# Kernel optimization log

Hardware: AMD Instinct MI355X
Metric: run time of the kernel (lower is better)

## Reference

```python
import jax, jax.numpy as jnp
import numpy as np

N, M, K, C, FF, H, OUT = 20000, 80000, 48, 64, 256, 4, 64


def _lin(x, w, b):
    return x @ w.T + b


def _bn(x, g, b, eps=1e-5):
    mu = x.mean(0)
    var = x.var(0)
    return (x - mu) * jax.lax.rsqrt(var + eps) * g + b


def setup_inputs() -> dict:
    key = jax.random.key(0)
    ks = jax.random.split(key, 24)
    voxel_features = jax.random.normal(ks[0], (M, C), jnp.float32)
    voxel_coords = jax.random.normal(ks[1], (M, 3), jnp.float32)
    query_coords = jax.random.normal(ks[2], (N, 3), jnp.float32)
    idx = jax.random.randint(ks[3], (N, K), 0, M)
    drop = jax.random.uniform(ks[4], (N, K)) < 0.1
    drop = drop.at[:, 0].set(False)  # keep >=1 valid key per query
    key_indices = jnp.where(drop, -1, idx)
    s = 0.05
    p = lambda i, shp: jax.random.normal(ks[i], shp, jnp.float32) * s
    return {
        "voxel_features": voxel_features,
        "voxel_coords": voxel_coords,
        "query_coords": query_coords,
        "key_indices": key_indices,
        "q_w": p(5, (C, 3)), "q_b": p(6, (C,)),
        "kpos_w": p(7, (C, 3)), "kpos_b": p(8, (C,)),
        "in_w": p(9, (3 * C, C)), "in_b": p(10, (3 * C,)),
        "out_w": p(11, (C, C)), "out_b": p(12, (C,)),
        "lin1_w": p(13, (FF, C)), "lin1_b": p(14, (FF,)),
        "lin2_w": p(15, (C, FF)), "lin2_b": p(16, (C,)),
        "norm_g": jnp.ones((C,), jnp.float32), "norm_b": jnp.zeros((C,), jnp.float32),
        "outl_w": p(17, (OUT, C)), "outl_b": p(18, (OUT,)),
        "obn_g": jnp.ones((OUT,), jnp.float32), "obn_b": jnp.zeros((OUT,), jnp.float32),
    }


def reference(voxel_features, voxel_coords, query_coords, key_indices,
              q_w, q_b, kpos_w, kpos_b, in_w, in_b, out_w, out_b,
              lin1_w, lin1_b, lin2_w, lin2_b, norm_g, norm_b,
              outl_w, outl_b, obn_g, obn_b):
    hd = C // H
    mask = key_indices < 0                      # (N,K) padded keys
    safe = jnp.where(mask, 0, key_indices)
    key_feats = voxel_features[safe]            # (N,K,C) hash-gather
    key_coords = voxel_coords[safe]             # (N,K,3)
    # query positional projection
    q_feat = jax.nn.relu(_lin(query_coords, q_w, q_b))          # (N,C)
    # relative coords + key positional conv1d(kernel=1) == linear on coord dim
    rel = key_coords - query_coords[:, None, :]                  # (N,K,3)
    key_feats = key_feats + jax.nn.relu(_lin(rel, kpos_w, kpos_b))
    # multihead attention, query length 1 per voxel
    Wq, Wk, Wv = jnp.split(in_w, 3, axis=0)
    bq, bk, bv = jnp.split(in_b, 3)
    q = (_lin(q_feat, Wq, bq) / jnp.sqrt(jnp.float32(hd))).reshape(N, H, hd)
    k = _lin(key_feats, Wk, bk).reshape(N, K, H, hd)
    v = _lin(key_feats, Wv, bv).reshape(N, K, H, hd)
    scores = jnp.einsum('nhd,nkhd->nhk', q, k)
    scores = jnp.where(mask[:, None, :], -jnp.inf, scores)
    attn = jax.nn.softmax(scores, axis=-1)
    ctx = jnp.einsum('nhk,nkhd->nhd', attn, v).reshape(N, C)
    att = _lin(ctx, out_w, out_b)                                # (N,C)
    # FFN + residual
    x = att + _lin(jax.nn.relu(_lin(att, lin1_w, lin1_b)), lin2_w, lin2_b)
    x = _bn(x, norm_g, norm_b)
    # output layer: Linear -> BN -> ReLU
    x = jax.nn.relu(_bn(_lin(x, outl_w, outl_b), obn_g, obn_b))
    return x
```

## Files before the change

kernel.cpp:

```cpp
#include <hip/hip_runtime.h>
#include <math.h>

#define N_Q 20000
#define KK 48
#define CC 64
#define FFD 256

#define TW_WOB   0
#define TW_WVT   4096
#define TW_L1B   8192
#define TW_L2B   16384
#define TW_OLB   24576
#define TW_QB    26624
#define TW_KB    28672
#define ST_OFF   32768
#define M_OFF    33024
#define VF_OFF   2593024
#define CTX_OFF  5153024

typedef short bf16x8 __attribute__((ext_vector_type(8)));
typedef float f32x4  __attribute__((ext_vector_type(4)));

__device__ __forceinline__ unsigned pk2(float a, float b) {
    unsigned r;
    asm("v_cvt_pk_bf16_f32 %0, %1, %2" : "=v"(r) : "v"(a), "v"(b));
    return r;
}
__device__ __forceinline__ unsigned f2bf(float a) {
    unsigned r;
    asm("v_cvt_pk_bf16_f32 %0, %1, 0" : "=v"(r) : "v"(a));
    return r & 0xffffu;
}
__device__ __forceinline__ float bflo(unsigned u) { return __uint_as_float(u << 16); }
__device__ __forceinline__ float bfhi(unsigned u) { return __uint_as_float(u & 0xffff0000u); }
__device__ __forceinline__ bf16x8 ldfrag(const unsigned short* p) {
    return *(const bf16x8*)p;
}

__global__ void prep_all(const float* __restrict__ in_w,
                         const float* __restrict__ out_w,
                         const float* __restrict__ lin1_w,
                         const float* __restrict__ lin2_w,
                         const float* __restrict__ outl_w,
                         const float* __restrict__ vfeat,
                         float* __restrict__ tw,
                         unsigned short* __restrict__ vfeat_bf,
                         float* __restrict__ stats)
{
    int t = blockIdx.x * 256 + threadIdx.x;
    unsigned* twu = (unsigned*)tw;
    if (t < 1280000) {
        float4 v = ((const float4*)vfeat)[t];
        uint2 p; p.x = pk2(v.x, v.y); p.y = pk2(v.z, v.w);
        ((uint2*)vfeat_bf)[t] = p;
    }
    if (t < 256) stats[t] = 0.0f;
    if (t < 4096) {
        if (t < 2048) {
            int p = t;
            int j2 = p & 3, lane = (p >> 2) & 63, nb = (p >> 8) & 3, ks = p >> 10;
            int nn = nb*16 + (lane & 15), k = ks*32 + (lane >> 4)*8 + 2*j2;
            twu[TW_WOB + p] = pk2(out_w[nn*64 + k], out_w[nn*64 + k + 1]);
        }
    } else if (t < 8192) {
        if (t < 6144) {
            int p = t - 4096;
            int j2 = p & 3, lane = (p >> 2) & 63, nb = (p >> 8) & 3, ks = p >> 10;
            int nn = nb*16 + (lane & 15), k = ks*32 + (lane >> 4)*8 + 2*j2;
            twu[TW_WVT + p] = pk2(in_w[(128 + nn)*64 + k], in_w[(128 + nn)*64 + k + 1]);
        }
    } else if (t < 16384) {
        int p = t - 8192;
        int j2 = p & 3, lane = (p >> 2) & 63, nb = (p >> 8) & 15, ks = p >> 12;
        int n = nb*16 + (lane & 15), k = ks*32 + (lane >> 4)*8 + 2*j2;
        twu[TW_L1B + p] = pk2(lin1_w[n*64 + k], lin1_w[n*64 + k + 1]);
    } else if (t < 24576) {
        int p = t - 16384;
        int j2 = p & 3, lane = (p >> 2) & 63, nb = (p >> 8) & 3, ks = p >> 10;
        int n = nb*16 + (lane & 15), k = ks*32 + (lane >> 4)*8 + 2*j2;
        twu[TW_L2B + p] = pk2(lin2_w[n*256 + k], lin2_w[n*256 + k + 1]);
    } else if (t < 26624) {
        int p = t - 24576;
        int j2 = p & 3, lane = (p >> 2) & 63, nb = (p >> 8) & 3, ks = p >> 10;
        int n = nb*16 + (lane & 15), k = ks*32 + (lane >> 4)*8 + 2*j2;
        twu[TW_OLB + p] = pk2(outl_w[n*64 + k], outl_w[n*64 + k + 1]);
    } else if (t < 28672) {
        int p = t - 26624;
        int j2 = p & 3, lane = (p >> 2) & 63, nb = (p >> 8) & 3, ks = p >> 10;
        int n = nb*16 + (lane & 15), k = ks*32 + (lane >> 4)*8 + 2*j2;
        twu[TW_QB + p] = pk2(in_w[n*64 + k], in_w[n*64 + k + 1]);
    } else if (t < 32768) {
        int p = t - 28672;
        int j2 = p & 3, lane = (p >> 2) & 63, nb = (p >> 8) & 3, h = p >> 10;
        int j = nb*16 + (lane & 15), k = (lane >> 4)*8 + 2*j2;
        unsigned u = 0;
        if (k < 16)
            u = pk2(in_w[(64 + h*16 + k)*64 + j], in_w[(64 + h*16 + k + 1)*64 + j]);
        twu[TW_KB + p] = u;
    }
}

__global__ __launch_bounds__(256) void m_kernel(
    const float* __restrict__ qcoord, const float* __restrict__ q_w,
    const float* __restrict__ q_b, const float* __restrict__ in_b,
    const float* __restrict__ tw, unsigned short* __restrict__ M_all)
{
    __shared__ __align__(16) unsigned short sQF[80*72];
    __shared__ __align__(16) unsigned short sQ[80*72];
    int t = threadIdx.x, base = blockIdx.x * 80;
    int colq = (t*4) & 63;
    float qwv[12];
    #pragma unroll
    for (int j = 0; j < 12; ++j) qwv[j] = q_w[colq*3 + j];
    float4 qb4 = *(const float4*)&q_b[colq];
    #pragma unroll
    for (int i = 0; i < 5; ++i) {
        int e = i*1024 + t*4, r = e >> 6, n = base + r;
        float c0 = qcoord[n*3], c1 = qcoord[n*3+1], c2 = qcoord[n*3+2];
        float f0 = fmaxf(fmaf(qwv[2],  c2, fmaf(qwv[1],  c1, fmaf(qwv[0], c0, qb4.x))), 0.f);
        float f1 = fmaxf(fmaf(qwv[5],  c2, fmaf(qwv[4],  c1, fmaf(qwv[3], c0, qb4.y))), 0.f);
        float f2 = fmaxf(fmaf(qwv[8],  c2, fmaf(qwv[7],  c1, fmaf(qwv[6], c0, qb4.z))), 0.f);
        float f3 = fmaxf(fmaf(qwv[11], c2, fmaf(qwv[10], c1, fmaf(qwv[9], c0, qb4.w))), 0.f);
        uint2 p; p.x = pk2(f0, f1); p.y = pk2(f2, f3);
        *(uint2*)&sQF[r*72 + colq] = p;
    }
    int w = t >> 6, lane = t & 63, l16 = lane & 15, quad = lane >> 4;
    const unsigned* QB = (const unsigned*)(tw + TW_QB);
    const unsigned* KB = (const unsigned*)(tw + TW_KB);
    bf16x8 qbf[2], kbf[4];
    #pragma unroll
    for (int ks = 0; ks < 2; ++ks)
        qbf[ks] = ldfrag((const unsigned short*)&QB[((ks*4 + w)*64 + lane)*4]);
    #pragma unroll
    for (int nb = 0; nb < 4; ++nb)
        kbf[nb] = ldfrag((const unsigned short*)&KB[((w*4 + nb)*64 + lane)*4]);
    __syncthreads();

    int cq = w*16 + l16;
    float bq = in_b[cq];
    #pragma unroll
    for (int mb = 0; mb < 5; ++mb) {
        bf16x8 a0 = ldfrag(&sQF[(mb*16 + l16)*72 + quad*8]);
        bf16x8 a1 = ldfrag(&sQF[(mb*16 + l16)*72 + 32 + quad*8]);
        f32x4 acc = {0.f, 0.f, 0.f, 0.f};
        acc = __builtin_amdgcn_mfma_f32_16x16x32_bf16(a0, qbf[0], acc, 0, 0, 0);
        acc = __builtin_amdgcn_mfma_f32_16x16x32_bf16(a1, qbf[1], acc, 0, 0, 0);
        #pragma unroll
        for (int reg = 0; reg < 4; ++reg) {
            int row = mb*16 + quad*4 + reg;
            sQ[row*72 + cq] = (unsigned short)f2bf((acc[reg] + bq) * 0.25f);
        }
    }
    #pragma unroll
    for (int mb = 0; mb < 5; ++mb) {
        bf16x8 a = {0,0,0,0,0,0,0,0};
        if (quad < 2) a = ldfrag(&sQ[(mb*16 + l16)*72 + w*16 + quad*8]);
        f32x4 acc[4];
        #pragma unroll
        for (int nb = 0; nb < 4; ++nb) {
            f32x4 z = {0.f, 0.f, 0.f, 0.f};
            acc[nb] = __builtin_amdgcn_mfma_f32_16x16x32_bf16(a, kbf[nb], z, 0, 0, 0);
        }
        #pragma unroll
        for (int nb = 0; nb < 4; ++nb)
            #pragma unroll
            for (int reg = 0; reg < 4; ++reg) {
                int r = base + mb*16 + quad*4 + reg, j = nb*16 + l16;
                M_all[(size_t)r*256 + w*64 + j] = (unsigned short)f2bf(acc[nb][reg]);
            }
    }
}

__global__ __launch_bounds__(256, 4) void attn_kernel(
    const unsigned short* __restrict__ vfeat_bf, const float* __restrict__ vcoord,
    const float* __restrict__ qcoord, const int* __restrict__ kidx,
    const float* __restrict__ kpos_w, const float* __restrict__ kpos_b,
    const float* __restrict__ in_b,
    const float* __restrict__ tw, const unsigned short* __restrict__ M_all,
    unsigned short* __restrict__ ctx_bf)
{
    __shared__ __align__(16) unsigned short skf2[4][KK*72];
    int wv = threadIdx.x >> 6, c = threadIdx.x & 63;
    int n = blockIdx.x * 4 + wv;
    unsigned short* skf = skf2[wv];
    int l16 = c & 15, quad = c >> 4;

    const unsigned short* Mrow = M_all + (size_t)n*256 + (l16 & 3)*64 + quad*8;
    bf16x8 mf0 = ldfrag(Mrow);
    bf16x8 mf1 = ldfrag(Mrow + 32);
    const unsigned* VBu = (const unsigned*)(tw + TW_WVT);
    bf16x8 wvf[2][4];
    #pragma unroll
    for (int ks = 0; ks < 2; ++ks)
        #pragma unroll
        for (int nb = 0; nb < 4; ++nb)
            wvf[ks][nb] = ldfrag((const unsigned short*)&VBu[((ks*4 + nb)*64 + c)*4]);

    float qc0 = qcoord[n*3+0], qc1 = qcoord[n*3+1], qc2 = qcoord[n*3+2];

    int kread = c < 48 ? c : 47;
    int idxv = kidx[(size_t)n*KK + kread];
    int sfe = idxv < 0 ? 0 : idxv;
    float rl0 = vcoord[sfe*3+0] - qc0;
    float rl1 = vcoord[sfe*3+1] - qc1;
    float rl2 = vcoord[sfe*3+2] - qc2;

    int o8 = c >> 3, jb8 = (c & 7) * 8;
    float w8[24], b8[8];
    #pragma unroll
    for (int q = 0; q < 6; ++q)
        *(float4*)&w8[q*4] = *(const float4*)(kpos_w + jb8*3 + q*4);
    *(float4*)&b8[0] = *(const float4*)(kpos_b + jb8);
    *(float4*)&b8[4] = *(const float4*)(kpos_b + jb8 + 4);

    uint4 fv[6];
    #pragma unroll
    for (int i = 0; i < 6; ++i) {
        int row = 8*i + o8;
        int si = __shfl(idxv, row);
        si = si < 0 ? 0 : si;
        fv[i] = *(const uint4*)(vfeat_bf + (size_t)si*64 + jb8);
    }
    #pragma unroll
    for (int i = 0; i < 6; ++i) {
        int row = 8*i + o8;
        float rr0 = __shfl(rl0, row), rr1 = __shfl(rl1, row), rr2 = __shfl(rl2, row);
        unsigned uu[4] = {fv[i].x, fv[i].y, fv[i].z, fv[i].w};
        unsigned pp[4];
        #pragma unroll
        for (int q2 = 0; q2 < 4; ++q2) {
            int k0 = 2*q2, k1 = 2*q2 + 1;
            float gl = bflo(uu[q2]), gh = bfhi(uu[q2]);
            gl += fmaxf(fmaf(w8[3*k0+2], rr2, fmaf(w8[3*k0+1], rr1, fmaf(w8[3*k0], rr0, b8[k0]))), 0.f);
            gh += fmaxf(fmaf(w8[3*k1+2], rr2, fmaf(w8[3*k1+1], rr1, fmaf(w8[3*k1], rr0, b8[k1]))), 0.f);
            pp[q2] = pk2(gl, gh);
        }
        uint4 st; st.x = pp[0]; st.y = pp[1]; st.z = pp[2]; st.w = pp[3];
        *(uint4*)&skf[row*72 + jb8] = st;
    }

    unsigned long long vm = __ballot(c < 48 && idxv >= 0);
    unsigned vmw = (unsigned)(vm >> (wv & 1 ? 0 : 0));
    bf16x8 a0s[3], a1s[3];
    float S[3][4];
    #pragma unroll
    for (int mb = 0; mb < 3; ++mb) {
        a0s[mb] = ldfrag(&skf[(mb*16 + l16)*72 + quad*8]);
        a1s[mb] = ldfrag(&skf[(mb*16 + l16)*72 + 32 + quad*8]);
        f32x4 acc = {0.f, 0.f, 0.f, 0.f};
        acc = __builtin_amdgcn_mfma_f32_16x16x32_bf16(a0s[mb], mf0, acc, 0, 0, 0);
        acc = __builtin_amdgcn_mfma_f32_16x16x32_bf16(a1s[mb], mf1, acc, 0, 0, 0);
        #pragma unroll
        for (int r = 0; r < 4; ++r) {
            int kk = mb*16 + quad*4 + r;
            S[mb][r] = ((vm >> kk) & 1ull) ? acc[r] : -1e30f;
        }
    }
    (void)vmw;

    float mx = S[0][0];
    #pragma unroll
    for (int mb = 0; mb < 3; ++mb)
        #pragma unroll
        for (int r = 0; r < 4; ++r) mx = fmaxf(mx, S[mb][r]);
    mx = fmaxf(mx, __shfl_xor(mx, 16));
    mx = fmaxf(mx, __shfl_xor(mx, 32));
    float p[3][4], es = 0.f;
    #pragma unroll
    for (int mb = 0; mb < 3; ++mb)
        #pragma unroll
        for (int r = 0; r < 4; ++r) { p[mb][r] = __expf(S[mb][r] - mx); es += p[mb][r]; }
    es += __shfl_xor(es, 16);
    es += __shfl_xor(es, 32);
    float rinv = 1.0f / es;
    #pragma unroll
    for (int mb = 0; mb < 3; ++mb)
        #pragma unroll
        for (int r = 0; r < 4; ++r) p[mb][r] *= rinv;

    float cacc0 = 0.f, cacc1 = 0.f, cacc2 = 0.f, cacc3 = 0.f;
    #pragma unroll
    for (int mb = 0; mb < 3; ++mb) {
        f32x4 av[4];
        #pragma unroll
        for (int nb = 0; nb < 4; ++nb) {
            f32x4 z = {0.f, 0.f, 0.f, 0.f};
            z = __builtin_amdgcn_mfma_f32_16x16x32_bf16(a0s[mb], wvf[0][nb], z, 0, 0, 0);
            av[nb] = __builtin_amdgcn_mfma_f32_16x16x32_bf16(a1s[mb], wvf[1][nb], z, 0, 0, 0);
        }
        #pragma unroll
        for (int r = 0; r < 4; ++r) {
            float pv = p[mb][r];
            float p0 = __shfl(pv, quad*16 + 0);
            float p1 = __shfl(pv, quad*16 + 1);
            float p2 = __shfl(pv, quad*16 + 2);
            float p3 = __shfl(pv, quad*16 + 3);
            cacc0 = fmaf(p0, av[0][r], cacc0);
            cacc1 = fmaf(p1, av[1][r], cacc1);
            cacc2 = fmaf(p2, av[2][r], cacc2);
            cacc3 = fmaf(p3, av[3][r], cacc3);
        }
    }
    cacc0 += __shfl_xor(cacc0, 16); cacc0 += __shfl_xor(cacc0, 32);
    cacc1 += __shfl_xor(cacc1, 16); cacc1 += __shfl_xor(cacc1, 32);
    cacc2 += __shfl_xor(cacc2, 16); cacc2 += __shfl_xor(cacc2, 32);
    cacc3 += __shfl_xor(cacc3, 16); cacc3 += __shfl_xor(cacc3, 32);
    float cv = quad == 0 ? cacc0 : quad == 1 ? cacc1 : quad == 2 ? cacc2 : cacc3;
    cv += in_b[128 + c];
    ctx_bf[(size_t)n*64 + c] = (unsigned short)f2bf(cv);
}

__global__ __launch_bounds__(256) void ffn_kernel(
    const float* __restrict__ tw, const float* __restrict__ out_b,
    const float* __restrict__ lin1_b, const float* __restrict__ lin2_b,
    const unsigned short* __restrict__ ctx_bf, float* __restrict__ y_out,
    float* __restrict__ sum1, float* __restrict__ sumsq1)
{
    __shared__ __align__(16) unsigned short sA[80*72];
    __shared__ __align__(16) unsigned short sH[80*264];
    int t = threadIdx.x, base = blockIdx.x * 80;
    int w = t >> 6, lane = t & 63, l16 = lane & 15, quad = lane >> 4;
    const unsigned* WOB = (const unsigned*)(tw + TW_WOB);
    const unsigned* L1B = (const unsigned*)(tw + TW_L1B);
    const unsigned* L2B = (const unsigned*)(tw + TW_L2B);
    bf16x8 wob[2], b1f[2][4], b2f[8];
    #pragma unroll
    for (int ks = 0; ks < 2; ++ks)
        wob[ks] = ldfrag((const unsigned short*)&WOB[((ks*4 + w)*64 + lane)*4]);
    #pragma unroll
    for (int ks = 0; ks < 2; ++ks)
        #pragma unroll
        for (int nb = 0; nb < 4; ++nb)
            b1f[ks][nb] = ldfrag((const unsigned short*)&L1B[((ks*16 + w*4 + nb)*64 + lane)*4]);
    #pragma unroll
    for (int ks = 0; ks < 8; ++ks)
        b2f[ks] = ldfrag((const unsigned short*)&L2B[((ks*4 + w)*64 + lane)*4]);

    int c = w*16 + l16;
    float ob = out_b[c];
    f32x4 attacc[5];
    #pragma unroll
    for (int mb = 0; mb < 5; ++mb) {
        const unsigned short* crow = ctx_bf + (size_t)(base + mb*16 + l16)*64;
        bf16x8 a0 = ldfrag(crow + quad*8);
        bf16x8 a1 = ldfrag(crow + 32 + quad*8);
        f32x4 acc = {0.f, 0.f, 0.f, 0.f};
        acc = __builtin_amdgcn_mfma_f32_16x16x32_bf16(a0, wob[0], acc, 0, 0, 0);
        acc = __builtin_amdgcn_mfma_f32_16x16x32_bf16(a1, wob[1], acc, 0, 0, 0);
        #pragma unroll
        for (int reg = 0; reg < 4; ++reg) {
            float av = acc[reg] + ob;
            attacc[mb][reg] = av;
            int row = mb*16 + quad*4 + reg;
            sA[row*72 + c] = (unsigned short)f2bf(av);
        }
    }
    __syncthreads();

    #pragma unroll
    for (int mb = 0; mb < 5; ++mb) {
        bf16x8 a0 = ldfrag(&sA[(mb*16 + l16)*72 + quad*8]);
        bf16x8 a1 = ldfrag(&sA[(mb*16 + l16)*72 + 32 + quad*8]);
        #pragma unroll
        for (int nb = 0; nb < 4; ++nb) {
            f32x4 acc = {0.f, 0.f, 0.f, 0.f};
            acc = __builtin_amdgcn_mfma_f32_16x16x32_bf16(a0, b1f[0][nb], acc, 0, 0, 0);
            acc = __builtin_amdgcn_mfma_f32_16x16x32_bf16(a1, b1f[1][nb], acc, 0, 0, 0);
            int f = w*64 + nb*16 + l16;
            float bias = lin1_b[f];
            #pragma unroll
            for (int reg = 0; reg < 4; ++reg) {
                int row = mb*16 + quad*4 + reg;
                sH[row*264 + f] = (unsigned short)f2bf(fmaxf(acc[reg] + bias, 0.0f));
            }
        }
    }
    __syncthreads();

    float lb2 = lin2_b[c];
    float s = 0.f, ss = 0.f;
    #pragma unroll
    for (int mb = 0; mb < 5; ++mb) {
        f32x4 acc = {0.f, 0.f, 0.f, 0.f};
        #pragma unroll
        for (int ks = 0; ks < 8; ++ks) {
            bf16x8 a = ldfrag(&sH[(mb*16 + l16)*264 + ks*32 + quad*8]);
            acc = __builtin_amdgcn_mfma_f32_16x16x32_bf16(a, b2f[ks], acc, 0, 0, 0);
        }
        #pragma unroll
        for (int reg = 0; reg < 4; ++reg) {
            int r = base + mb*16 + quad*4 + reg;
            float y = attacc[mb][reg] + lb2 + acc[reg];
            y_out[(size_t)r*64 + c] = y;
            s += y; ss = fmaf(y, y, ss);
        }
    }
    s  += __shfl_xor(s, 16);  s  += __shfl_xor(s, 32);
    ss += __shfl_xor(ss, 16); ss += __shfl_xor(ss, 32);
    if (lane < 16) {
        atomicAdd(&sum1[c], s);
        atomicAdd(&sumsq1[c], ss);
    }
}

__global__ __launch_bounds__(256) void linout_kernel(
    const float* __restrict__ tw, const float* __restrict__ outl_b,
    const float* __restrict__ norm_g, const float* __restrict__ norm_b,
    const float* __restrict__ sum1, const float* __restrict__ sumsq1,
    const float* __restrict__ y, float* __restrict__ z_out,
    float* __restrict__ sum2, float* __restrict__ sumsq2)
{
    __shared__ __align__(16) unsigned short sX[80*72];
    int t = threadIdx.x, base = blockIdx.x * 80;
    int colq = (t*4) & 63;
    const float invN = 1.0f / 20000.0f;
    float4 sm = *(const float4*)&sum1[colq];
    float4 sq = *(const float4*)&sumsq1[colq];
    float4 g  = *(const float4*)&norm_g[colq];
    float4 bb = *(const float4*)&norm_b[colq];
    float mu0 = sm.x*invN, mu1 = sm.y*invN, mu2 = sm.z*invN, mu3 = sm.w*invN;
    float a0 = g.x / sqrtf(fmaf(-mu0, mu0, sq.x*invN) + 1e-5f);
    float a1 = g.y / sqrtf(fmaf(-mu1, mu1, sq.y*invN) + 1e-5f);
    float a2 = g.z / sqrtf(fmaf(-mu2, mu2, sq.z*invN) + 1e-5f);
    float a3 = g.w / sqrtf(fmaf(-mu3, mu3, sq.w*invN) + 1e-5f);
    float b0 = fmaf(-mu0, a0, bb.x), b1 = fmaf(-mu1, a1, bb.y);
    float b2 = fmaf(-mu2, a2, bb.z), b3 = fmaf(-mu3, a3, bb.w);
    #pragma unroll
    for (int i = 0; i < 5; ++i) {
        int e = i*1024 + t*4, r = e >> 6;
        float4 v = *(const float4*)&y[(size_t)(base + r)*64 + colq];
        uint2 p;
        p.x = pk2(fmaf(v.x, a0, b0), fmaf(v.y, a1, b1));
        p.y = pk2(fmaf(v.z, a2, b2), fmaf(v.w, a3, b3));
        *(uint2*)&sX[r*72 + colq] = p;
    }
    int w = t >> 6, lane = t & 63, l16 = lane & 15, quad = lane >> 4;
    const unsigned* OLB = (const unsigned*)(tw + TW_OLB);
    bf16x8 obf[2];
    #pragma unroll
    for (int ks = 0; ks < 2; ++ks)
        obf[ks] = ldfrag((const unsigned short*)&OLB[((ks*4 + w)*64 + lane)*4]);
    __syncthreads();

    int co = w*16 + l16;
    float ob = outl_b[co];
    float s = 0.f, ss = 0.f;
    #pragma unroll
    for (int mb = 0; mb < 5; ++mb) {
        bf16x8 x0 = ldfrag(&sX[(mb*16 + l16)*72 + quad*8]);
        bf16x8 x1 = ldfrag(&sX[(mb*16 + l16)*72 + 32 + quad*8]);
        f32x4 acc = {0.f, 0.f, 0.f, 0.f};
        acc = __builtin_amdgcn_mfma_f32_16x16x32_bf16(x0, obf[0], acc, 0, 0, 0);
        acc = __builtin_amdgcn_mfma_f32_16x16x32_bf16(x1, obf[1], acc, 0, 0, 0);
        #pragma unroll
        for (int reg = 0; reg < 4; ++reg) {
            int r = base + mb*16 + quad*4 + reg;
            float zv = acc[reg] + ob;
            z_out[(size_t)r*64 + co] = zv;
            s += zv; ss = fmaf(zv, zv, ss);
        }
    }
    s  += __shfl_xor(s, 16);  s  += __shfl_xor(s, 32);
    ss += __shfl_xor(ss, 16); ss += __shfl_xor(ss, 32);
    if (lane < 16) {
        atomicAdd(&sum2[co], s);
        atomicAdd(&sumsq2[co], ss);
    }
}

__global__ void final_kernel(float* __restrict__ z,
    const float* __restrict__ sum2, const float* __restrict__ sumsq2,
    const float* __restrict__ obn_g, const float* __restrict__ obn_b)
{
    int i = blockIdx.x*blockDim.x + threadIdx.x;
    if (i >= N_Q*64/4) return;
    int o4 = (i*4) & 63;
    float4 sm = *(const float4*)&sum2[o4];
    float4 sq = *(const float4*)&sumsq2[o4];
    float4 g  = *(const float4*)&obn_g[o4];
    float4 b  = *(const float4*)&obn_b[o4];
    const float invN = 1.0f / 20000.0f;
    float mux = sm.x*invN, muy = sm.y*invN, muz = sm.z*invN, muw = sm.w*invN;
    float ax = g.x / sqrtf(fmaf(-mux, mux, sq.x*invN) + 1e-5f);
    float ay = g.y / sqrtf(fmaf(-muy, muy, sq.y*invN) + 1e-5f);
    float az = g.z / sqrtf(fmaf(-muz, muz, sq.z*invN) + 1e-5f);
    float aw = g.w / sqrtf(fmaf(-muw, muw, sq.w*invN) + 1e-5f);
    float4 v = ((float4*)z)[i];
    v.x = fmaxf(fmaf(v.x - mux, ax, b.x), 0.0f);
    v.y = fmaxf(fmaf(v.y - muy, ay, b.y), 0.0f);
    v.z = fmaxf(fmaf(v.z - muz, az, b.z), 0.0f);
    v.w = fmaxf(fmaf(v.w - muw, aw, b.w), 0.0f);
    ((float4*)z)[i] = v;
}

extern "C" void kernel_launch(void* const* d_in, const int* in_sizes, int n_in,
                              void* d_out, int out_size, void* d_ws, size_t ws_size,
                              hipStream_t stream)
{
    const float* vfeat  = (const float*)d_in[0];
    const float* vcoord = (const float*)d_in[1];
    const float* qcoord = (const float*)d_in[2];
    const int*   kidx   = (const int*)d_in[3];
    const float* q_w    = (const float*)d_in[4];
    const float* q_b    = (const float*)d_in[5];
    const float* kpos_w = (const float*)d_in[6];
    const float* kpos_b = (const float*)d_in[7];
    const float* in_w   = (const float*)d_in[8];
    const float* in_b   = (const float*)d_in[9];
    const float* out_w  = (const float*)d_in[10];
    const float* out_b  = (const float*)d_in[11];
    const float* lin1_w = (const float*)d_in[12];
    const float* lin1_b = (const float*)d_in[13];
    const float* lin2_w = (const float*)d_in[14];
    const float* lin2_b = (const float*)d_in[15];
    const float* norm_g = (const float*)d_in[16];
    const float* norm_b = (const float*)d_in[17];
    const float* outl_w = (const float*)d_in[18];
    const float* outl_b = (const float*)d_in[19];
    const float* obn_g  = (const float*)d_in[20];
    const float* obn_b  = (const float*)d_in[21];

    float* ws = (float*)d_ws;
    float* tw = ws;
    float* stats = ws + ST_OFF;
    float* sum1 = stats, *sumsq1 = stats + 64, *sum2 = stats + 128, *sumsq2 = stats + 192;
    unsigned short* M_all = (unsigned short*)(ws + M_OFF);
    unsigned short* vfeat_bf = (unsigned short*)(ws + VF_OFF);
    unsigned short* ctx_bf = (unsigned short*)(ws + CTX_OFF);
    float* xd = (float*)d_out;

    prep_all<<<5120, 256, 0, stream>>>(in_w, out_w, lin1_w, lin2_w, outl_w,
                                       vfeat, tw, vfeat_bf, stats);
    m_kernel<<<250, 256, 0, stream>>>(qcoord, q_w, q_b, in_b, tw, M_all);
    attn_kernel<<<N_Q/4, 256, 0, stream>>>(vfeat_bf, vcoord, qcoord, kidx, kpos_w,
                                           kpos_b, in_b, tw, M_all, ctx_bf);
    ffn_kernel<<<250, 256, 0, stream>>>(tw, out_b, lin1_b, lin2_b, ctx_bf, xd,
                                        sum1, sumsq1);
    linout_kernel<<<250, 256, 0, stream>>>(tw, outl_b, norm_g, norm_b, sum1, sumsq1,
                                           xd, xd, sum2, sumsq2);
    final_kernel<<<1250, 256, 0, stream>>>(xd, sum2, sumsq2, obn_g, obn_b);
}
```

Baseline: 170.2 us.

## Merge prep and M kernels, swizzle attention LDS, raise attn occupancy

Merges the weight and feature prep kernel with the query-projection M kernel into one launch. Extra blocks do the conversion work, and the M blocks now build their Q and K weight fragments straight from fp32 in_w instead of reading pre-packed copies, which removes a launch and a dependency. The attention kernel's LDS key tile drops its 72-element padded stride for a 64-element stride with an XOR swizzle. This shrinks shared memory while avoiding bank conflicts, and launch bounds go from 4 to 6 waves-per-SIMD hints to raise occupancy, at the risk of register spills.

```diff
diff --git a/kernel.cpp b/kernel.cpp
--- a/kernel.cpp
+++ b/kernel.cpp
@@ -11,8 +11,6 @@
 #define TW_L1B   8192
 #define TW_L2B   16384
 #define TW_OLB   24576
-#define TW_QB    26624
-#define TW_KB    28672
 #define ST_OFF   32768
 #define M_OFF    33024
 #define VF_OFF   2593024
@@ -36,77 +34,62 @@
 __device__ __forceinline__ bf16x8 ldfrag(const unsigned short* p) {
     return *(const bf16x8*)p;
 }
-
-__global__ void prep_all(const float* __restrict__ in_w,
-                         const float* __restrict__ out_w,
-                         const float* __restrict__ lin1_w,
-                         const float* __restrict__ lin2_w,
-                         const float* __restrict__ outl_w,
-                         const float* __restrict__ vfeat,
-                         float* __restrict__ tw,
-                         unsigned short* __restrict__ vfeat_bf,
-                         float* __restrict__ stats)
-{
-    int t = blockIdx.x * 256 + threadIdx.x;
-    unsigned* twu = (unsigned*)tw;
-    if (t < 1280000) {
-        float4 v = ((const float4*)vfeat)[t];
-        uint2 p; p.x = pk2(v.x, v.y); p.y = pk2(v.z, v.w);
-        ((uint2*)vfeat_bf)[t] = p;
-    }
-    if (t < 256) stats[t] = 0.0f;
-    if (t < 4096) {
-        if (t < 2048) {
-            int p = t;
-            int j2 = p & 3, lane = (p >> 2) & 63, nb = (p >> 8) & 3, ks = p >> 10;
-            int nn = nb*16 + (lane & 15), k = ks*32 + (lane >> 4)*8 + 2*j2;
-            twu[TW_WOB + p] = pk2(out_w[nn*64 + k], out_w[nn*64 + k + 1]);
-        }
-    } else if (t < 8192) {
-        if (t < 6144) {
-            int p = t - 4096;
-            int j2 = p & 3, lane = (p >> 2) & 63, nb = (p >> 8) & 3, ks = p >> 10;
-            int nn = nb*16 + (lane & 15), k = ks*32 + (lane >> 4)*8 + 2*j2;
-            twu[TW_WVT + p] = pk2(in_w[(128 + nn)*64 + k], in_w[(128 + nn)*64 + k + 1]);
-        }
-    } else if (t < 16384) {
-        int p = t - 8192;
-        int j2 = p & 3, lane = (p >> 2) & 63, nb = (p >> 8) & 15, ks = p >> 12;
-        int n = nb*16 + (lane & 15), k = ks*32 + (lane >> 4)*8 + 2*j2;
-        twu[TW_L1B + p] = pk2(lin1_w[n*64 + k], lin1_w[n*64 + k + 1]);
-    } else if (t < 24576) {
-        int p = t - 16384;
-        int j2 = p & 3, lane = (p >> 2) & 63, nb = (p >> 8) & 3, ks = p >> 10;
-        int n = nb*16 + (lane & 15), k = ks*32 + (lane >> 4)*8 + 2*j2;
-        twu[TW_L2B + p] = pk2(lin2_w[n*256 + k], lin2_w[n*256 + k + 1]);
-    } else if (t < 26624) {
-        int p = t - 24576;
-        int j2 = p & 3, lane = (p >> 2) & 63, nb = (p >> 8) & 3, ks = p >> 10;
-        int n = nb*16 + (lane & 15), k = ks*32 + (lane >> 4)*8 + 2*j2;
-        twu[TW_OLB + p] = pk2(outl_w[n*64 + k], outl_w[n*64 + k + 1]);
-    } else if (t < 28672) {
-        int p = t - 26624;
-        int j2 = p & 3, lane = (p >> 2) & 63, nb = (p >> 8) & 3, ks = p >> 10;
-        int n = nb*16 + (lane & 15), k = ks*32 + (lane >> 4)*8 + 2*j2;
-        twu[TW_QB + p] = pk2(in_w[n*64 + k], in_w[n*64 + k + 1]);
-    } else if (t < 32768) {
-        int p = t - 28672;
-        int j2 = p & 3, lane = (p >> 2) & 63, nb = (p >> 8) & 3, h = p >> 10;
-        int j = nb*16 + (lane & 15), k = (lane >> 4)*8 + 2*j2;
-        unsigned u = 0;
-        if (k < 16)
-            u = pk2(in_w[(64 + h*16 + k)*64 + j], in_w[(64 + h*16 + k + 1)*64 + j]);
-        twu[TW_KB + p] = u;
-    }
-}
-
-__global__ __launch_bounds__(256) void m_kernel(
+union U84 { unsigned u[4]; bf16x8 v; };
+
+__global__ __launch_bounds__(256) void prep_m(
+    const float* __restrict__ in_w, const float* __restrict__ out_w,
+    const float* __restrict__ lin1_w, const float* __restrict__ lin2_w,
+    const float* __restrict__ outl_w, const float* __restrict__ vfeat,
     const float* __restrict__ qcoord, const float* __restrict__ q_w,
     const float* __restrict__ q_b, const float* __restrict__ in_b,
-    const float* __restrict__ tw, unsigned short* __restrict__ M_all)
+    float* __restrict__ tw, unsigned short* __restrict__ vfeat_bf,
+    float* __restrict__ stats, unsigned short* __restrict__ M_all)
 {
     __shared__ __align__(16) unsigned short sQF[80*72];
     __shared__ __align__(16) unsigned short sQ[80*72];
+
+    if (blockIdx.x >= 250) {
+        int t = (blockIdx.x - 250) * 256 + threadIdx.x;
+        unsigned* twu = (unsigned*)tw;
+        if (t < 1280000) {
+            float4 v = ((const float4*)vfeat)[t];
+            uint2 p; p.x = pk2(v.x, v.y); p.y = pk2(v.z, v.w);
+            ((uint2*)vfeat_bf)[t] = p;
+        }
+        if (t < 256) stats[t] = 0.0f;
+        if (t < 4096) {
+            if (t < 2048) {
+                int p = t;
+                int j2 = p & 3, lane = (p >> 2) & 63, nb = (p >> 8) & 3, ks = p >> 10;
+                int nn = nb*16 + (lane & 15), k = ks*32 + (lane >> 4)*8 + 2*j2;
+                twu[TW_WOB + p] = pk2(out_w[nn*64 + k], out_w[nn*64 + k + 1]);
+            }
+        } else if (t < 8192) {
+            if (t < 6144) {
+                int p = t - 4096;
+                int j2 = p & 3, lane = (p >> 2) & 63, nb = (p >> 8) & 3, ks = p >> 10;
+                int nn = nb*16 + (lane & 15), k = ks*32 + (lane >> 4)*8 + 2*j2;
+                twu[TW_WVT + p] = pk2(in_w[(128 + nn)*64 + k], in_w[(128 + nn)*64 + k + 1]);
+            }
+        } else if (t < 16384) {
+            int p = t - 8192;
+            int j2 = p & 3, lane = (p >> 2) & 63, nb = (p >> 8) & 15, ks = p >> 12;
+            int n = nb*16 + (lane & 15), k = ks*32 + (lane >> 4)*8 + 2*j2;
+            twu[TW_L1B + p] = pk2(lin1_w[n*64 + k], lin1_w[n*64 + k + 1]);
+        } else if (t < 24576) {
+            int p = t - 16384;
+            int j2 = p & 3, lane = (p >> 2) & 63, nb = (p >> 8) & 3, ks = p >> 10;
+            int n = nb*16 + (lane & 15), k = ks*32 + (lane >> 4)*8 + 2*j2;
+            twu[TW_L2B + p] = pk2(lin2_w[n*256 + k], lin2_w[n*256 + k + 1]);
+        } else if (t < 26624) {
+            int p = t - 24576;
+            int j2 = p & 3, lane = (p >> 2) & 63, nb = (p >> 8) & 3, ks = p >> 10;
+            int n = nb*16 + (lane & 15), k = ks*32 + (lane >> 4)*8 + 2*j2;
+            twu[TW_OLB + p] = pk2(outl_w[n*64 + k], outl_w[n*64 + k + 1]);
+        }
+        return;
+    }
+
     int t = threadIdx.x, base = blockIdx.x * 80;
     int colq = (t*4) & 63;
     float qwv[12];
@@ -125,15 +108,35 @@
         *(uint2*)&sQF[r*72 + colq] = p;
     }
     int w = t >> 6, lane = t & 63, l16 = lane & 15, quad = lane >> 4;
-    const unsigned* QB = (const unsigned*)(tw + TW_QB);
-    const unsigned* KB = (const unsigned*)(tw + TW_KB);
     bf16x8 qbf[2], kbf[4];
-    #pragma unroll
-    for (int ks = 0; ks < 2; ++ks)
-        qbf[ks] = ldfrag((const unsigned short*)&QB[((ks*4 + w)*64 + lane)*4]);
-    #pragma unroll
-    for (int nb = 0; nb < 4; ++nb)
-        kbf[nb] = ldfrag((const unsigned short*)&KB[((w*4 + nb)*64 + lane)*4]);
+    {
+        const float* qrow = in_w + (w*16 + l16)*64;
+        #pragma unroll
+        for (int ks = 0; ks < 2; ++ks) {
+            float4 aa = *(const float4*)&qrow[ks*32 + quad*8];
+            float4 bb = *(const float4*)&qrow[ks*32 + quad*8 + 4];
+            U84 u;
+            u.u[0] = pk2(aa.x, aa.y); u.u[1] = pk2(aa.z, aa.w);
+            u.u[2] = pk2(bb.x, bb.y); u.u[3] = pk2(bb.z, bb.w);
+            qbf[ks] = u.v;
+        }
+        #pragma unroll
+        for (int nb = 0; nb < 4; ++nb) {
+            U84 u;
+            if (quad < 2) {
+                int jj = nb*16 + l16;
+                #pragma unroll
+                for (int j2 = 0; j2 < 4; ++j2) {
+                    int k = quad*8 + 2*j2;
+                    u.u[j2] = pk2(in_w[(64 + w*16 + k)*64 + jj],
+                                  in_w[(64 + w*16 + k + 1)*64 + jj]);
+                }
+            } else {
+                u.u[0] = u.u[1] = u.u[2] = u.u[3] = 0;
+            }
+            kbf[nb] = u.v;
+        }
+    }
     __syncthreads();
 
     int cq = w*16 + l16;
@@ -171,7 +174,7 @@
     }
 }
 
-__global__ __launch_bounds__(256, 4) void attn_kernel(
+__global__ __launch_bounds__(256, 6) void attn_kernel(
     const unsigned short* __restrict__ vfeat_bf, const float* __restrict__ vcoord,
     const float* __restrict__ qcoord, const int* __restrict__ kidx,
     const float* __restrict__ kpos_w, const float* __restrict__ kpos_b,
@@ -179,7 +182,7 @@
     const float* __restrict__ tw, const unsigned short* __restrict__ M_all,
     unsigned short* __restrict__ ctx_bf)
 {
-    __shared__ __align__(16) unsigned short skf2[4][KK*72];
+    __shared__ __align__(16) unsigned short skf2[4][KK*64];
     int wv = threadIdx.x >> 6, c = threadIdx.x & 63;
     int n = blockIdx.x * 4 + wv;
     unsigned short* skf = skf2[wv];
@@ -236,17 +239,17 @@
             pp[q2] = pk2(gl, gh);
         }
         uint4 st; st.x = pp[0]; st.y = pp[1]; st.z = pp[2]; st.w = pp[3];
-        *(uint4*)&skf[row*72 + jb8] = st;
+        *(uint4*)&skf[row*64 + (jb8 ^ ((row & 7) << 3))] = st;
     }
 
     unsigned long long vm = __ballot(c < 48 && idxv >= 0);
-    unsigned vmw = (unsigned)(vm >> (wv & 1 ? 0 : 0));
     bf16x8 a0s[3], a1s[3];
     float S[3][4];
     #pragma unroll
     for (int mb = 0; mb < 3; ++mb) {
-        a0s[mb] = ldfrag(&skf[(mb*16 + l16)*72 + quad*8]);
-        a1s[mb] = ldfrag(&skf[(mb*16 + l16)*72 + 32 + quad*8]);
+        int r0 = mb*16 + l16, sw = (l16 & 7) << 3;
+        a0s[mb] = ldfrag(&skf[r0*64 + ((quad*8) ^ sw)]);
+        a1s[mb] = ldfrag(&skf[r0*64 + ((32 + quad*8) ^ sw)]);
         f32x4 acc = {0.f, 0.f, 0.f, 0.f};
         acc = __builtin_amdgcn_mfma_f32_16x16x32_bf16(a0s[mb], mf0, acc, 0, 0, 0);
         acc = __builtin_amdgcn_mfma_f32_16x16x32_bf16(a1s[mb], mf1, acc, 0, 0, 0);
@@ -256,7 +259,6 @@
             S[mb][r] = ((vm >> kk) & 1ull) ? acc[r] : -1e30f;
         }
     }
-    (void)vmw;
 
     float mx = S[0][0];
     #pragma unroll
@@ -529,9 +531,9 @@
     unsigned short* ctx_bf = (unsigned short*)(ws + CTX_OFF);
     float* xd = (float*)d_out;
 
-    prep_all<<<5120, 256, 0, stream>>>(in_w, out_w, lin1_w, lin2_w, outl_w,
-                                       vfeat, tw, vfeat_bf, stats);
-    m_kernel<<<250, 256, 0, stream>>>(qcoord, q_w, q_b, in_b, tw, M_all);
+    prep_m<<<5370, 256, 0, stream>>>(in_w, out_w, lin1_w, lin2_w, outl_w, vfeat,
+                                     qcoord, q_w, q_b, in_b, tw, vfeat_bf,
+                                     stats, M_all);
     attn_kernel<<<N_Q/4, 256, 0, stream>>>(vfeat_bf, vcoord, qcoord, kidx, kpos_w,
                                            kpos_b, in_b, tw, M_all, ctx_bf);
     ffn_kernel<<<250, 256, 0, stream>>>(tw, out_b, lin1_b, lin2_b, ctx_bf, xd,
```

New measurement: 214.5 us. +26.0%, slower.
